# Performance work log

Hardware: AMD Instinct MI355X
Metric: run time of the kernel (lower is better)

## Reference

```python
import jax, jax.numpy as jnp
import numpy as np


def setup_inputs() -> dict:
    key = jax.random.key(0)
    ks = jax.random.split(key, 7)
    B, S = 64, 1024
    V, E, H, L, O = 128, 512, 512, 2, 256
    scale = 0.05
    return {
        "input_ids": jax.random.randint(ks[0], (B, S), 0, V),
        "emb": jax.random.normal(ks[1], (V, E), dtype=jnp.float32) * scale,
        "Wxh": jax.random.normal(ks[2], (L, H, E), dtype=jnp.float32) * scale,
        "Whh": jax.random.normal(ks[3], (L, H, H), dtype=jnp.float32) * scale,
        "bh": jax.random.normal(ks[4], (L, H), dtype=jnp.float32) * scale,
        "Why": jax.random.normal(ks[5], (O, H), dtype=jnp.float32) * scale,
        "by": jax.random.normal(ks[6], (O,), dtype=jnp.float32) * scale,
    }


def reference(input_ids, emb, Wxh, Whh, bh, Why, by):
    # input_ids: [B, S] int; emb: [V, E]; Wxh/Whh: [L, H, *]; bh: [L, H]
    L, H, _ = Wxh.shape
    B, S = input_ids.shape
    embedded = emb[input_ids]                 # [B, S, E]
    xs = jnp.swapaxes(embedded, 0, 1)         # [S, B, E] for scan over time
    h0 = jnp.zeros((L, B, H), dtype=embedded.dtype)

    def step(h, x_t):
        inp = x_t
        new_h = []
        for l in range(L):  # small fixed layer loop
            hn = jnp.tanh(inp @ Wxh[l].T + h[l] @ Whh[l].T + bh[l])
            new_h.append(hn)
            inp = hn
        return jnp.stack(new_h), inp          # carry [L,B,H], emit top layer [B,H]

    _, ys = jax.lax.scan(step, h0, xs)        # ys: [S, B, H]
    hidden_seq = jnp.swapaxes(ys, 0, 1)       # [B, S, H]
    return hidden_seq @ Why.T + by            # [B, S, O]
```

## Files before the change

### kernel.cpp

```cpp
#include <hip/hip_runtime.h>
#include <stdint.h>

#define B_ 64
#define S_ 1024
#define V_ 128
#define E_ 512
#define H_ 512
#define O_ 256
#define PSLOT (B_ * H_ * 2)

typedef __attribute__((ext_vector_type(8))) short bf16x8;
typedef __attribute__((ext_vector_type(4))) float f32x4;
typedef __attribute__((ext_vector_type(4))) unsigned int u32x4;
typedef __attribute__((ext_vector_type(2))) unsigned int u32x2;
typedef unsigned short u16;
typedef unsigned int u32;

__device__ __forceinline__ u16 f2bf(float f) {
  unsigned u = __builtin_bit_cast(unsigned, f);
  u = u + 0x7FFFu + ((u >> 16) & 1u);
  return (u16)(u >> 16);
}
__device__ __forceinline__ float bf2f(u16 h) {
  unsigned u = ((unsigned)h) << 16;
  return __builtin_bit_cast(float, u);
}
__device__ __forceinline__ float fast_tanh(float x) {
  float a = __builtin_amdgcn_exp2f(x * 2.8853900817779268f);
  return 1.0f - 2.0f * __builtin_amdgcn_rcpf(a + 1.0f);
}
__device__ __forceinline__ u32 pk_hi(u32 a, u32 b) { return (a & 0xffffu) | (b << 16); }
__device__ __forceinline__ u32 pk_lo(u32 a, u32 b) { return (a >> 16) | (b & 0xffff0000u); }

__device__ __forceinline__ u32x4 ld_sc1_x4(const u32* p) {
  u32x4 v;
  asm volatile("global_load_dwordx4 %0, %1, off sc0 sc1" : "=v"(v) : "v"(p));
  return v;
}
__device__ __forceinline__ u32x2 ld_sc1_x2(const u32* p) {
  u32x2 v;
  asm volatile("global_load_dwordx2 %0, %1, off sc0 sc1" : "=v"(v) : "v"(p));
  return v;
}
__device__ __forceinline__ void st_sc1_x2(u32* p, u32 d, u32 tag) {
  u32x2 v = {d, tag};
  asm volatile("global_store_dwordx2 %0, %1, off sc0 sc1" :: "v"(p), "v"(v) : "memory");
}
__device__ __forceinline__ void st_sc1_u32(u32* p, u32 v) {
  asm volatile("global_store_dword %0, %1, off sc0 sc1" :: "v"(p), "v"(v) : "memory");
}
__device__ __forceinline__ void st_short_nt(u16* p, u32 v) {
  asm volatile("global_store_short %0, %1, off nt" :: "v"(p), "v"(v) : "memory");
}
__device__ __forceinline__ void vm0_fence() {
  asm volatile("s_waitcnt vmcnt(0)" ::: "memory");
  __builtin_amdgcn_sched_barrier(0);
}
__device__ __forceinline__ void poll4(const u32* p, u32 tgt) {
  for (;;) {
    u32x4 v;
    asm volatile("global_load_dwordx4 %0, %1, off sc0 sc1\n\ts_waitcnt vmcnt(0)"
                 : "=v"(v) : "v"(p) : "memory");
    if (v.x >= tgt && v.y >= tgt && v.z >= tgt && v.w >= tgt) return;
    __builtin_amdgcn_s_sleep(1);
  }
}

__global__ void k_embed(const float* __restrict__ emb, const float* __restrict__ Wxh0,
                        const float* __restrict__ bh0, float* __restrict__ EW0) {
  __shared__ float es[E_];
  const int v = blockIdx.x;
  for (int e = threadIdx.x; e < E_; e += blockDim.x) es[e] = emb[v * E_ + e];
  __syncthreads();
  for (int h = threadIdx.x; h < H_; h += blockDim.x) {
    const float* wr = Wxh0 + (size_t)h * E_;
    float acc = bh0[h];
    #pragma unroll 4
    for (int e = 0; e < E_; e += 4)
      acc += es[e] * wr[e] + es[e+1] * wr[e+1] + es[e+2] * wr[e+2] + es[e+3] * wr[e+3];
    EW0[(size_t)v * H_ + h] = acc;
  }
}

__global__ __launch_bounds__(512, 2) void k_pipe(
    const float* __restrict__ Whh, const float* __restrict__ Wxh,
    const int* __restrict__ ids, const float* __restrict__ EW0,
    const float* __restrict__ bh,
    u32* __restrict__ h0r,
    u32* __restrict__ x1r,
    u32* __restrict__ h1r,
    u16* __restrict__ h1full,
    u32* __restrict__ fa)
{
  __shared__ u32 lds_hi_w[2 * 4096];
  __shared__ u32 lds_lo_w[2 * 4096];

  const int tid  = threadIdx.x;
  const int wave = tid >> 6, lane = tid & 63;
  const int l15 = lane & 15, lhi = lane >> 4;
  const int bid = blockIdx.x;
  const int role = bid >> 4, sub = bid & 15;
  const int g = sub >> 2, cb = sub & 3;
  const int n = cb * 128 + wave * 16 + l15;

  u32* x1prog = fa;
  u32* r2prog = fa + 16;

  const float* Wsel = (role == 0) ? Whh
                    : (role == 1) ? (Wxh + (size_t)H_ * H_)
                                  : (Whh + (size_t)H_ * H_);
  bf16x8 whi[16], wlo[16];
  {
    const float* wr = Wsel + (size_t)n * H_ + lhi * 8;
    #pragma unroll
    for (int ks = 0; ks < 16; ++ks) {
      const float* src = wr + ks * 32;
      bf16x8 h, l;
      #pragma unroll
      for (int j = 0; j < 8; ++j) {
        const float v = src[j];
        const u16 hb = f2bf(v);
        h[j] = (short)hb;
        l[j] = (short)f2bf(v - bf2f(hb));
      }
      whi[ks] = h; wlo[ks] = l;
    }
  }

  int aoff[16];
  {
    const int sw = l15 & 7;
    #pragma unroll
    for (int ks = 0; ks < 16; ++ks)
      aoff[ks] = l15 * 1024 + (((ks * 4 + lhi) ^ sw) << 4);
  }

  const int sr = tid >> 5, sm = tid & 31;
  const int rowbase = (g * 16 + sr) * 512;

  auto wr_lds = [&](int buf, int cs, u32 d0, u32 d1, u32 d2, u32 d3) {
    const int byte = buf * 16384 + sr * 1024 + (sm & 1) * 8 +
                     ((((cs << 4) + (sm >> 1)) ^ (sr & 7)) << 4);
    u32x2 hi = { pk_hi(d0, d1), pk_hi(d2, d3) };
    u32x2 lo = { pk_lo(d0, d1), pk_lo(d2, d3) };
    *(u32x2*)((char*)lds_hi_w + byte) = hi;
    *(u32x2*)((char*)lds_lo_w + byte) = lo;
  };

  auto pollstage3 = [&](const u32* slot, u32 want, int buf) {
    const int c0 = (cb + 1) & 3, c1 = (cb + 2) & 3, c2 = (cb + 3) & 3;
    const u32* p0 = slot + ((rowbase + c0 * 128 + sm * 4) << 1);
    const u32* p1 = slot + ((rowbase + c1 * 128 + sm * 4) << 1);
    const u32* p2 = slot + ((rowbase + c2 * 128 + sm * 4) << 1);
    u32x4 a0, a1, b0, b1, d0, d1;
    for (;;) {
      a0 = ld_sc1_x4(p0); a1 = ld_sc1_x4(p0 + 4);
      b0 = ld_sc1_x4(p1); b1 = ld_sc1_x4(p1 + 4);
      d0 = ld_sc1_x4(p2); d1 = ld_sc1_x4(p2 + 4);
      vm0_fence();
      u32 bad = (a0.y ^ want) | (a0.w ^ want) | (a1.y ^ want) | (a1.w ^ want)
              | (b0.y ^ want) | (b0.w ^ want) | (b1.y ^ want) | (b1.w ^ want)
              | (d0.y ^ want) | (d0.w ^ want) | (d1.y ^ want) | (d1.w ^ want);
      if (!bad) break;
    }
    wr_lds(buf, c0, a0.x, a0.z, a1.x, a1.z);
    wr_lds(buf, c1, b0.x, b0.z, b1.x, b1.z);
    wr_lds(buf, c2, d0.x, d0.z, d1.x, d1.z);
  };

  auto pollstage4 = [&](const u32* slot, u32 want, int buf) {
    const u32* p0 = slot + ((rowbase + sm * 4) << 1);
    u32x4 q[8];
    for (;;) {
      #pragma unroll
      for (int c = 0; c < 4; ++c) {
        q[2*c]   = ld_sc1_x4(p0 + (c * 128 << 1));
        q[2*c+1] = ld_sc1_x4(p0 + (c * 128 << 1) + 4);
      }
      vm0_fence();
      u32 bad = 0;
      #pragma unroll
      for (int i = 0; i < 8; ++i) bad |= (q[i].y ^ want) | (q[i].w ^ want);
      if (!bad) break;
    }
    #pragma unroll
    for (int c = 0; c < 4; ++c)
      wr_lds(buf, c, q[2*c].x, q[2*c].z, q[2*c+1].x, q[2*c+1].z);
  };

  auto mm3 = [&](int buf, f32x4& out) {
    const char* bh_ = (const char*)lds_hi_w + buf * 16384;
    const char* bl_ = (const char*)lds_lo_w + buf * 16384;
    f32x4 c0 = {0.f,0.f,0.f,0.f}, c1 = c0, c2 = c0;
    #pragma unroll
    for (int ks = 0; ks < 16; ++ks) {
      bf16x8 ah = *(const bf16x8*)(bh_ + aoff[ks]);
      bf16x8 al = *(const bf16x8*)(bl_ + aoff[ks]);
      c0 = __builtin_amdgcn_mfma_f32_16x16x32_bf16(ah, whi[ks], c0, 0, 0, 0);
      c1 = __builtin_amdgcn_mfma_f32_16x16x32_bf16(al, whi[ks], c1, 0, 0, 0);
      c2 = __builtin_amdgcn_mfma_f32_16x16x32_bf16(ah, wlo[ks], c2, 0, 0, 0);
    }
    out = c0 + c1 + c2;
  };

  auto self_write = [&](int buf, const u16* hbv, const u16* lbv) {
    char* bh_ = (char*)lds_hi_w + buf * 16384;
    char* bl_ = (char*)lds_lo_w + buf * 16384;
    const int gcol = n >> 3, coff = (n & 7) * 2;
    #pragma unroll
    for (int j = 0; j < 4; ++j) {
      const int r = lhi * 4 + j;
      const int byte = r * 1024 + ((gcol ^ (r & 7)) << 4) + coff;
      *(u16*)(bh_ + byte) = hbv[j];
      *(u16*)(bl_ + byte) = lbv[j];
    }
  };

  if (role == 0) {
    for (int t = 0; t < S_; ++t) {
      float ew[4];
      #pragma unroll
      for (int j = 0; j < 4; ++j) {
        const int b = g * 16 + lhi * 4 + j;
        ew[j] = EW0[(size_t)ids[b * S_ + t] * H_ + n];
      }
      const int cur = t & 1;
      f32x4 acc = {0.f,0.f,0.f,0.f};
      if (t > 0) mm3(cur, acc);
      u32* wsl = h0r + (size_t)(t & 15) * PSLOT;
      u16 hbv[4], lbv[4];
      #pragma unroll
      for (int j = 0; j < 4; ++j) {
        const int b = g * 16 + lhi * 4 + j;
        const float h = fast_tanh(acc[j] + ew[j]);
        hbv[j] = f2bf(h);
        lbv[j] = f2bf(h - bf2f(hbv[j]));
        st_sc1_x2(wsl + (((size_t)b * 512 + n) << 1),
                  (u32)hbv[j] | ((u32)lbv[j] << 16), (u32)(t + 1));
      }
      self_write(cur ^ 1, hbv, lbv);
      if ((t & 7) == 0 && t >= 16 && tid == 0) poll4(&x1prog[g * 4], (u32)(t - 8));
      if (t + 1 < S_) pollstage3(wsl, (u32)(t + 1), cur ^ 1);
      __syncthreads();
    }
  } else if (role == 1) {
    const float bias = bh[H_ + n];
    for (int t = 0; t < S_; ++t) {
      if ((t & 7) == 0 && t >= 16 && tid == 0) poll4(&r2prog[g * 4], (u32)(t - 8));
      const int cur = t & 1;
      pollstage4(h0r + (size_t)(t & 15) * PSLOT, (u32)(t + 1), cur);
      __syncthreads();
      f32x4 acc;
      mm3(cur, acc);
      u32* xsl = x1r + (size_t)(t & 15) * PSLOT;
      #pragma unroll
      for (int j = 0; j < 4; ++j) {
        const int b = g * 16 + lhi * 4 + j;
        const float v = acc[j] + bias;
        st_sc1_x2(xsl + (((size_t)b * 512 + n) << 1),
                  __builtin_bit_cast(u32, v), (u32)(t + 1));
      }
      if ((t & 7) == 7 && tid == 0) st_sc1_u32(&x1prog[g * 4 + cb], (u32)(t + 1));
    }
  } else {
    u32 xvb[4];
    {
      const u32* xsl = x1r;
      u32x2 xq[4];
      for (;;) {
        #pragma unroll
        for (int j = 0; j < 4; ++j) {
          const int b = g * 16 + lhi * 4 + j;
          xq[j] = ld_sc1_x2(xsl + (((size_t)b * 512 + n) << 1));
        }
        vm0_fence();
        u32 bad = 0;
        #pragma unroll
        for (int j = 0; j < 4; ++j) bad |= xq[j].y ^ 1u;
        if (!bad) break;
      }
      #pragma unroll
      for (int j = 0; j < 4; ++j) xvb[j] = xq[j].x;
    }
    for (int t = 0; t < S_; ++t) {
      const int cur = t & 1;
      f32x4 acc = {0.f,0.f,0.f,0.f};
      if (t > 0) mm3(cur, acc);
      u32* wsl = h1r + (size_t)(t & 3) * PSLOT;
      u16 hbv[4], lbv[4];
      #pragma unroll
      for (int j = 0; j < 4; ++j) {
        const int b = g * 16 + lhi * 4 + j;
        const float h = fast_tanh(acc[j] + __builtin_bit_cast(float, xvb[j]));
        hbv[j] = f2bf(h);
        lbv[j] = f2bf(h - bf2f(hbv[j]));
        st_sc1_x2(wsl + (((size_t)b * 512 + n) << 1),
                  (u32)hbv[j] | ((u32)lbv[j] << 16), (u32)(t + 1));
        st_short_nt(h1full + ((size_t)b * S_ + t) * H_ + n, (u32)hbv[j]);
      }
      self_write(cur ^ 1, hbv, lbv);
      if ((t & 7) == 7 && tid == 0) st_sc1_u32(&r2prog[g * 4 + cb], (u32)(t + 1));
      if (t + 1 < S_) {
        const u32 want = (u32)(t + 1), xwant = (u32)(t + 2);
        const int c0 = (cb + 1) & 3, c1 = (cb + 2) & 3, c2 = (cb + 3) & 3;
        const u32* p0 = wsl + ((rowbase + c0 * 128 + sm * 4) << 1);
        const u32* p1 = wsl + ((rowbase + c1 * 128 + sm * 4) << 1);
        const u32* p2 = wsl + ((rowbase + c2 * 128 + sm * 4) << 1);
        const u32* xsl = x1r + (size_t)((t + 1) & 15) * PSLOT;
        u32x4 a0, a1, b0, b1, d0, d1;
        u32x2 xq[4];
        for (;;) {
          a0 = ld_sc1_x4(p0); a1 = ld_sc1_x4(p0 + 4);
          b0 = ld_sc1_x4(p1); b1 = ld_sc1_x4(p1 + 4);
          d0 = ld_sc1_x4(p2); d1 = ld_sc1_x4(p2 + 4);
          #pragma unroll
          for (int j = 0; j < 4; ++j) {
            const int b = g * 16 + lhi * 4 + j;
            xq[j] = ld_sc1_x2(xsl + (((size_t)b * 512 + n) << 1));
          }
          vm0_fence();
          u32 bad = (a0.y ^ want) | (a0.w ^ want) | (a1.y ^ want) | (a1.w ^ want)
                  | (b0.y ^ want) | (b0.w ^ want) | (b1.y ^ want) | (b1.w ^ want)
                  | (d0.y ^ want) | (d0.w ^ want) | (d1.y ^ want) | (d1.w ^ want);
          #pragma unroll
          for (int j = 0; j < 4; ++j) bad |= xq[j].y ^ xwant;
          if (!bad) break;
        }
        wr_lds(cur ^ 1, c0, a0.x, a0.z, a1.x, a1.z);
        wr_lds(cur ^ 1, c1, b0.x, b0.z, b1.x, b1.z);
        wr_lds(cur ^ 1, c2, d0.x, d0.z, d1.x, d1.z);
        #pragma unroll
        for (int j = 0; j < 4; ++j) xvb[j] = xq[j].x;
      }
      __syncthreads();
    }
  }
}

__global__ void k_gemm_out(const u16* __restrict__ A, const float* __restrict__ Bw,
                           const float* __restrict__ bias, float* __restrict__ outp) {
  const int tid  = threadIdx.x;
  const int wave = tid >> 6, lane = tid & 63;
  const int l15 = lane & 15, lhi = lane >> 4;
  const int M0  = blockIdx.x * 64;
  const int ncb = wave * 64;

  #pragma unroll
  for (int nt = 0; nt < 4; ++nt) {
    const int nn = ncb + nt * 16 + l15;
    const float* wr = Bw + (size_t)nn * H_ + lhi * 8;
    bf16x8 w[16];
    #pragma unroll
    for (int ks = 0; ks < 16; ++ks) {
      const float* src = wr + ks * 32;
      bf16x8 ww;
      #pragma unroll
      for (int j = 0; j < 8; ++j) ww[j] = (short)f2bf(src[j]);
      w[ks] = ww;
    }
    const float bs = bias[nn];
    for (int mi = 0; mi < 4; ++mi) {
      const int m0 = M0 + mi * 16;
      const u16* arow = A + ((size_t)(m0 + l15)) * H_ + lhi * 8;
      f32x4 acc = {0.f, 0.f, 0.f, 0.f};
      #pragma unroll
      for (int ks = 0; ks < 16; ++ks) {
        bf16x8 a = *(const bf16x8*)(arow + ks * 32);
        acc = __builtin_amdgcn_mfma_f32_16x16x32_bf16(a, w[ks], acc, 0, 0, 0);
      }
      #pragma unroll
      for (int j = 0; j < 4; ++j)
        outp[(size_t)(m0 + lhi * 4 + j) * O_ + nn] = acc[j] + bs;
    }
  }
}

extern "C" void kernel_launch(void* const* d_in, const int* in_sizes, int n_in,
                              void* d_out, int out_size, void* d_ws, size_t ws_size,
                              hipStream_t stream) {
  const int*   ids = (const int*)d_in[0];
  const float* emb = (const float*)d_in[1];
  const float* Wxh = (const float*)d_in[2];
  const float* Whh = (const float*)d_in[3];
  const float* bh  = (const float*)d_in[4];
  const float* Why = (const float*)d_in[5];
  const float* by  = (const float*)d_in[6];
  float* out = (float*)d_out;

  char* ws = (char*)d_ws;
  size_t off = 0;
  float* EW0  = (float*)(ws + off); off += (size_t)V_ * H_ * 4;
  u32* h0r    = (u32*)(ws + off);   off += (size_t)16 * PSLOT * 4;
  u32* x1r    = (u32*)(ws + off);   off += (size_t)16 * PSLOT * 4;
  u32* h1r    = (u32*)(ws + off);   off += (size_t)4 * PSLOT * 4;
  u32* fa     = (u32*)(ws + off);   off += 4096;
  u16* h1full = (u16*)(ws + off);   off += (size_t)B_ * S_ * H_ * 2;

  const size_t zlen = (size_t)(16 + 16 + 4) * PSLOT * 4 + 4096;
  hipMemsetAsync(h0r, 0, zlen, stream);

  k_embed<<<dim3(V_), dim3(256), 0, stream>>>(emb, Wxh, bh, EW0);

  k_pipe<<<dim3(48), dim3(512), 0, stream>>>(Whh, Wxh, ids, EW0, bh,
                                             h0r, x1r, h1r, h1full, fa);

  k_gemm_out<<<dim3((B_ * S_) / 64), dim3(256), 0, stream>>>(h1full, Why, by, out);
}
```

Baseline: 4.188 ms.

## Add per-step block flags so consumers poll one flag before bulk loads

Adds per-timestep, per-group readiness flags (h0f, h1f). Each producer block publishes its flag after a block barrier, and consumers spin on four flags from a single thread before doing the tagged data loads. The goal is to replace wide all-thread spinning on tagged payloads with cheap single-thread flag polling, which should cut memory traffic during waits. Role 1 also publishes its x1 progress earlier, and a sleep is added to the initial poll loop. In exchange, each step gains extra __syncthreads calls and a flag round trip on the serial recurrence path.

```diff
diff --git a/kernel.cpp b/kernel.cpp
--- a/kernel.cpp
+++ b/kernel.cpp
@@ -103,8 +103,10 @@
   const int g = sub >> 2, cb = sub & 3;
   const int n = cb * 128 + wave * 16 + l15;
 
-  u32* x1prog = fa;
-  u32* r2prog = fa + 16;
+  u32* h0f    = fa;
+  u32* h1f    = fa + 256;
+  u32* x1prog = fa + 512;
+  u32* r2prog = fa + 528;
 
   const float* Wsel = (role == 0) ? Whh
                     : (role == 1) ? (Wxh + (size_t)H_ * H_)
@@ -239,17 +241,29 @@
                   (u32)hbv[j] | ((u32)lbv[j] << 16), (u32)(t + 1));
       }
       self_write(cur ^ 1, hbv, lbv);
-      if ((t & 7) == 0 && t >= 16 && tid == 0) poll4(&x1prog[g * 4], (u32)(t - 8));
+      __syncthreads();
+      if (tid == 0) {
+        st_sc1_u32(&h0f[((g << 4) | (t & 15)) * 4 + cb], (u32)(t + 1));
+        if ((t & 7) == 0 && t >= 16) poll4(&x1prog[g * 4], (u32)(t - 8));
+        if (t + 1 < S_) poll4(&h0f[((g << 4) | (t & 15)) * 4], (u32)(t + 1));
+      }
+      __syncthreads();
       if (t + 1 < S_) pollstage3(wsl, (u32)(t + 1), cur ^ 1);
       __syncthreads();
     }
   } else if (role == 1) {
     const float bias = bh[H_ + n];
     for (int t = 0; t < S_; ++t) {
-      if ((t & 7) == 0 && t >= 16 && tid == 0) poll4(&r2prog[g * 4], (u32)(t - 8));
+      if (tid == 0) {
+        poll4(&h0f[((g << 4) | (t & 15)) * 4], (u32)(t + 1));
+        if ((t & 7) == 0 && t >= 16) poll4(&r2prog[g * 4], (u32)(t - 8));
+      }
+      __syncthreads();
       const int cur = t & 1;
       pollstage4(h0r + (size_t)(t & 15) * PSLOT, (u32)(t + 1), cur);
       __syncthreads();
+      if (tid == 0 && (t & 7) == 7)
+        st_sc1_u32(&x1prog[g * 4 + cb], (u32)(t + 1));
       f32x4 acc;
       mm3(cur, acc);
       u32* xsl = x1r + (size_t)(t & 15) * PSLOT;
@@ -260,24 +274,23 @@
         st_sc1_x2(xsl + (((size_t)b * 512 + n) << 1),
                   __builtin_bit_cast(u32, v), (u32)(t + 1));
       }
-      if ((t & 7) == 7 && tid == 0) st_sc1_u32(&x1prog[g * 4 + cb], (u32)(t + 1));
     }
   } else {
     u32 xvb[4];
     {
-      const u32* xsl = x1r;
       u32x2 xq[4];
       for (;;) {
         #pragma unroll
         for (int j = 0; j < 4; ++j) {
           const int b = g * 16 + lhi * 4 + j;
-          xq[j] = ld_sc1_x2(xsl + (((size_t)b * 512 + n) << 1));
+          xq[j] = ld_sc1_x2(x1r + (((size_t)b * 512 + n) << 1));
         }
         vm0_fence();
         u32 bad = 0;
         #pragma unroll
         for (int j = 0; j < 4; ++j) bad |= xq[j].y ^ 1u;
         if (!bad) break;
+        __builtin_amdgcn_s_sleep(1);
       }
       #pragma unroll
       for (int j = 0; j < 4; ++j) xvb[j] = xq[j].x;
@@ -299,36 +312,29 @@
         st_short_nt(h1full + ((size_t)b * S_ + t) * H_ + n, (u32)hbv[j]);
       }
       self_write(cur ^ 1, hbv, lbv);
-      if ((t & 7) == 7 && tid == 0) st_sc1_u32(&r2prog[g * 4 + cb], (u32)(t + 1));
+      __syncthreads();
+      if (tid == 0) {
+        st_sc1_u32(&h1f[((g << 4) | (t & 15)) * 4 + cb], (u32)(t + 1));
+        if ((t & 7) == 7) st_sc1_u32(&r2prog[g * 4 + cb], (u32)(t + 1));
+        if (t + 1 < S_) poll4(&h1f[((g << 4) | (t & 15)) * 4], (u32)(t + 1));
+      }
+      __syncthreads();
       if (t + 1 < S_) {
-        const u32 want = (u32)(t + 1), xwant = (u32)(t + 2);
-        const int c0 = (cb + 1) & 3, c1 = (cb + 2) & 3, c2 = (cb + 3) & 3;
-        const u32* p0 = wsl + ((rowbase + c0 * 128 + sm * 4) << 1);
-        const u32* p1 = wsl + ((rowbase + c1 * 128 + sm * 4) << 1);
-        const u32* p2 = wsl + ((rowbase + c2 * 128 + sm * 4) << 1);
+        pollstage3(wsl, (u32)(t + 1), cur ^ 1);
         const u32* xsl = x1r + (size_t)((t + 1) & 15) * PSLOT;
-        u32x4 a0, a1, b0, b1, d0, d1;
         u32x2 xq[4];
         for (;;) {
-          a0 = ld_sc1_x4(p0); a1 = ld_sc1_x4(p0 + 4);
-          b0 = ld_sc1_x4(p1); b1 = ld_sc1_x4(p1 + 4);
-          d0 = ld_sc1_x4(p2); d1 = ld_sc1_x4(p2 + 4);
           #pragma unroll
           for (int j = 0; j < 4; ++j) {
             const int b = g * 16 + lhi * 4 + j;
             xq[j] = ld_sc1_x2(xsl + (((size_t)b * 512 + n) << 1));
           }
           vm0_fence();
-          u32 bad = (a0.y ^ want) | (a0.w ^ want) | (a1.y ^ want) | (a1.w ^ want)
-                  | (b0.y ^ want) | (b0.w ^ want) | (b1.y ^ want) | (b1.w ^ want)
-                  | (d0.y ^ want) | (d0.w ^ want) | (d1.y ^ want) | (d1.w ^ want);
+          u32 bad = 0;
           #pragma unroll
-          for (int j = 0; j < 4; ++j) bad |= xq[j].y ^ xwant;
+          for (int j = 0; j < 4; ++j) bad |= xq[j].y ^ (u32)(t + 2);
           if (!bad) break;
         }
-        wr_lds(cur ^ 1, c0, a0.x, a0.z, a1.x, a1.z);
-        wr_lds(cur ^ 1, c1, b0.x, b0.z, b1.x, b1.z);
-        wr_lds(cur ^ 1, c2, d0.x, d0.z, d1.x, d1.z);
         #pragma unroll
         for (int j = 0; j < 4; ++j) xvb[j] = xq[j].x;
       }
```

New measurement: 4.275 ms. 1.02x slower.
